# Kernel tuning notes

Hardware: AMD Instinct MI355X
Metric: run time of the kernel (lower is better)

## Reference

```python
import jax, jax.numpy as jnp
import numpy as np

L, B, S, H, NH, HD = 2, 2, 1024, 768, 12, 64
E, K, F, V = 8, 2, 3072, 50257
THETA = 10000.0
EPS = 1e-5


def setup_inputs() -> dict:
    key = jax.random.key(0)
    ks = iter(jax.random.split(key, 40))
    def nrm(shape):
        return jax.random.normal(next(ks), shape, jnp.float32) * 0.02
    return {
        "input_ids": jax.random.randint(next(ks), (B, S), 0, V),
        "emb": nrm((V, H)),
        "ln1_w": jnp.ones((L, H)), "ln1_b": jnp.zeros((L, H)),
        "ln2_w": jnp.ones((L, H)), "ln2_b": jnp.zeros((L, H)),
        "lnf_w": jnp.ones((H,)), "lnf_b": jnp.zeros((H,)),
        "Wq": nrm((L, H, H)), "bq": jnp.zeros((L, H)),
        "Wk": nrm((L, H, H)), "bk": jnp.zeros((L, H)),
        "Wv": nrm((L, H, H)), "bv": jnp.zeros((L, H)),
        "Wo": nrm((L, H, H)), "bo": jnp.zeros((L, H)),
        "Wr": nrm((L, H, E)), "br": jnp.zeros((L, E)),
        "W1": nrm((L, E, H, F)), "b1": jnp.zeros((L, E, F)),
        "W2": nrm((L, E, F, H)), "b2": jnp.zeros((L, E, H)),
    }


def _layer_norm(x, w, b):
    m = x.mean(-1, keepdims=True)
    v = ((x - m) ** 2).mean(-1, keepdims=True)
    return (x - m) * jax.lax.rsqrt(v + EPS) * w + b


def _rotate_half(x):
    x1, x2 = jnp.split(x, 2, axis=-1)
    return jnp.concatenate([-x2, x1], axis=-1)


def _forward(input_ids, emb, ln1_w, ln1_b, ln2_w, ln2_b, lnf_w, lnf_b,
             Wq, bq, Wk, bk, Wv, bv, Wo, bo, Wr, br, W1, b1, W2, b2):
    x = emb[input_ids]  # [B,S,H]

    # RoPE tables [1,1,S,HD]
    inv_freq = 1.0 / (THETA ** (jnp.arange(0, HD, 2, dtype=jnp.float32) / HD))
    freqs = jnp.arange(S, dtype=jnp.float32)[:, None] * inv_freq[None, :]
    ang = jnp.concatenate([freqs, freqs], axis=-1)
    cos = jnp.cos(ang)[None, None].astype(x.dtype)
    sin = jnp.sin(ang)[None, None].astype(x.dtype)

    causal = jnp.where(jnp.tril(jnp.ones((S, S), dtype=bool)), 0.0, -1e9)
    causal = causal[None, None].astype(x.dtype)

    scale = 1.0 / np.sqrt(HD)
    for l in range(L):
        # --- attention block ---
        h = _layer_norm(x, ln1_w[l], ln1_b[l])
        q = (h @ Wq[l] + bq[l]).reshape(B, S, NH, HD).transpose(0, 2, 1, 3)
        k = (h @ Wk[l] + bk[l]).reshape(B, S, NH, HD).transpose(0, 2, 1, 3)
        v = (h @ Wv[l] + bv[l]).reshape(B, S, NH, HD).transpose(0, 2, 1, 3)
        q = q * cos + _rotate_half(q) * sin
        k = k * cos + _rotate_half(k) * sin
        scores = jnp.einsum('bhqd,bhkd->bhqk', q, k) * scale + causal
        attn = jax.nn.softmax(scores, axis=-1)
        o = jnp.einsum('bhqk,bhkd->bhqd', attn, v)
        o = o.transpose(0, 2, 1, 3).reshape(B, S, H)
        x = x + (o @ Wo[l] + bo[l])

        # --- MoE feed-forward block ---
        h = _layer_norm(x, ln2_w[l], ln2_b[l]).reshape(-1, H)  # [N,H]
        router_probs = jax.nn.softmax(h @ Wr[l] + br[l], axis=-1)  # [N,E]
        tp, ti = jax.lax.top_k(router_probs, K)
        tp = tp / (tp.sum(-1, keepdims=True) + 1e-9)
        # combine weights per expert (equiv. to the per-slot scatter loop)
        w = (jax.nn.one_hot(ti, E, dtype=h.dtype) * tp[..., None]).sum(1)  # [N,E]
        a = jax.nn.gelu(jnp.einsum('nh,ehf->nef', h, W1[l]) + b1[l], approximate=False)
        oe = jnp.einsum('nef,efh->neh', a, W2[l]) + b2[l]
        ff = jnp.einsum('ne,neh->nh', w, oe)
        x = x + ff.reshape(B, S, H)

    x = _layer_norm(x, lnf_w, lnf_b)
    logits = jnp.einsum('bsh,vh->bsv', x, emb)  # tied lm_head
    return logits


def reference(input_ids, emb, ln1_w, ln1_b, ln2_w, ln2_b, lnf_w, lnf_b,
              Wq, bq, Wk, bk, Wv, bv, Wo, bo, Wr, br, W1, b1, W2, b2):
    return _forward(input_ids, emb, ln1_w, ln1_b, ln2_w, ln2_b, lnf_w, lnf_b,
                    Wq, bq, Wk, bk, Wv, bv, Wo, bo, Wr, br, W1, b1, W2, b2)
```

## Files before the change

### kernel.cpp

```cpp
#include <hip/hip_runtime.h>
#include <stdint.h>

constexpr int L = 2, Bb = 2, S = 1024, H = 768, NHd = 12, HD = 64;
constexpr int E = 8, F = 3072, V = 50257;
constexpr int NTOK = Bb * S;
constexpr int NSLOT = NTOK * 2;
constexpr float EPSLN = 1e-5f;

typedef __attribute__((ext_vector_type(4))) float f32x4;
typedef __attribute__((ext_vector_type(8))) short s16x8;

#define DEVI __device__ __forceinline__

DEVI float bf2f(short u) {
  union { float f; uint32_t i; } c; c.i = ((uint32_t)(uint16_t)u) << 16; return c.f;
}
DEVI short f2bf(float f) {
  union { float f; uint32_t i; } c; c.f = f;
  uint32_t x = c.i;
  uint32_t r = (x + 0x7fffu + ((x >> 16) & 1u)) >> 16;
  return (short)r;
}

DEVI void gload16(const void* g, void* l) {
  __builtin_amdgcn_global_load_lds(g, l, 16, 0, 0);
}

DEVI float gelu1(float g) { return 0.5f * g * (1.f + erff(g * 0.70710678118f)); }

__global__ void k_f32_to_bf16(const float* __restrict__ in, short* __restrict__ out, long n4) {
  long i = (long)blockIdx.x * blockDim.x + threadIdx.x;
  if (i >= n4) return;
  long base = i * 4;
  f32x4 v = *(const f32x4*)(in + base);
  short4 o;
  o.x = f2bf(v.x); o.y = f2bf(v.y); o.z = f2bf(v.z); o.w = f2bf(v.w);
  *(short4*)(out + base) = o;
}

__global__ void k_transpose_bf16(const float* __restrict__ in, short* __restrict__ out,
                                 int R, int C, long inBS, long outBS) {
  __shared__ float tile[32][33];
  const float* src = in + (size_t)blockIdx.z * inBS;
  short* dst = out + (size_t)blockIdx.z * outBS;
  int r0 = blockIdx.y * 32, c0 = blockIdx.x * 32;
  int tx = threadIdx.x, ty = threadIdx.y;
#pragma unroll
  for (int i = 0; i < 32; i += 8) {
    int r = r0 + ty + i, c = c0 + tx;
    if (r < R && c < C) tile[ty + i][tx] = src[(size_t)r * C + c];
  }
  __syncthreads();
#pragma unroll
  for (int i = 0; i < 32; i += 8) {
    int c = c0 + ty + i, r = r0 + tx;
    if (r < R && c < C) dst[(size_t)c * R + r] = f2bf(tile[tx][ty + i]);
  }
}

__global__ void k_transpose_split(const float* __restrict__ in, short* __restrict__ oh,
                                  short* __restrict__ ol, int R, int C, long inBS,
                                  long outBS) {
  __shared__ float tile[32][33];
  const float* src = in + (size_t)blockIdx.z * inBS;
  short* dh = oh + (size_t)blockIdx.z * outBS;
  short* dl = ol + (size_t)blockIdx.z * outBS;
  int r0 = blockIdx.y * 32, c0 = blockIdx.x * 32;
  int tx = threadIdx.x, ty = threadIdx.y;
#pragma unroll
  for (int i = 0; i < 32; i += 8) {
    int r = r0 + ty + i, c = c0 + tx;
    if (r < R && c < C) tile[ty + i][tx] = src[(size_t)r * C + c];
  }
  __syncthreads();
#pragma unroll
  for (int i = 0; i < 32; i += 8) {
    int c = c0 + ty + i, r = r0 + tx;
    if (r < R && c < C) {
      float v = tile[tx][ty + i];
      short hi = f2bf(v);
      short lo = f2bf(v - bf2f(hi));
      dh[(size_t)c * R + r] = hi;
      dl[(size_t)c * R + r] = lo;
    }
  }
}

__global__ void k_wqkv_t2(const float* __restrict__ Wq, const float* __restrict__ Wk,
                          const float* __restrict__ Wv, short* __restrict__ o0,
                          short* __restrict__ o1) {
  __shared__ float tile[32][33];
  const int zz = blockIdx.z;
  const float* in = (zz == 0) ? Wq : (zz == 1) ? Wk : Wv;
  const size_t doff = (size_t)zz * H * H;
  int r0 = blockIdx.y * 32, c0 = blockIdx.x * 32;
  int tx = threadIdx.x, ty = threadIdx.y;
#pragma unroll
  for (int i = 0; i < 32; i += 8) {
    int r = r0 + ty + i, c = c0 + tx;
    tile[ty + i][tx] = in[(size_t)r * H + c];
  }
  __syncthreads();
#pragma unroll
  for (int i = 0; i < 32; i += 8) {
    int c = c0 + ty + i, r = r0 + tx;
    float v = tile[tx][ty + i];
    short t0 = f2bf(v);
    short t1 = f2bf(v - bf2f(t0));
    o0[doff + (size_t)c * H + r] = t0;
    o1[doff + (size_t)c * H + r] = t1;
  }
}

__global__ void k_bqkv(const float* __restrict__ bq, const float* __restrict__ bk,
                       const float* __restrict__ bv, float* __restrict__ bqkv) {
  int i = blockIdx.x * blockDim.x + threadIdx.x;
  if (i >= L * 3 * H) return;
  int l = i / (3 * H), j = i % (3 * H);
  float v = (j < H) ? bq[l * H + j] : (j < 2 * H) ? bk[l * H + j - H] : bv[l * H + j - 2 * H];
  bqkv[i] = v;
}

__global__ void k_ropetab(float* __restrict__ cosT, float* __restrict__ sinT) {
  int i = blockIdx.x * blockDim.x + threadIdx.x;
  if (i >= S * (HD / 2)) return;
  int s = i / 32, d = i % 32;
  float invf = powf(10000.f, -(2.f * d) / (float)HD);
  float ang = (float)s * invf;
  cosT[i] = cosf(ang);
  sinT[i] = sinf(ang);
}

__global__ void k_embed(const int* __restrict__ ids, const float* __restrict__ emb,
                        float* __restrict__ x) {
  int idx = blockIdx.x * blockDim.x + threadIdx.x;
  int row = idx / (H / 4), c4 = idx % (H / 4);
  if (row >= NTOK) return;
  int t = ids[row];
  ((f32x4*)(x + (size_t)row * H))[c4] = ((const f32x4*)(emb + (size_t)t * H))[c4];
}

template <int OUT>
__global__ void k_layernorm(const float* __restrict__ x, const float* __restrict__ w,
                            const float* __restrict__ b, float* __restrict__ of,
                            short* __restrict__ s0, short* __restrict__ s1) {
  int row = blockIdx.x * (blockDim.x >> 6) + (threadIdx.x >> 6);
  int lane = threadIdx.x & 63;
  if (row >= NTOK) return;
  const float* xr = x + (size_t)row * H;
  float v[12], s = 0.f, s2s = 0.f;
#pragma unroll
  for (int j = 0; j < 12; j++) { float t = xr[lane + j * 64]; v[j] = t; s += t; s2s += t * t; }
#pragma unroll
  for (int off = 32; off; off >>= 1) { s += __shfl_xor(s, off); s2s += __shfl_xor(s2s, off); }
  float m = s / (float)H;
  float var = s2s / (float)H - m * m;
  float rs = 1.f / sqrtf(var + EPSLN);
#pragma unroll
  for (int j = 0; j < 12; j++) {
    int c = lane + j * 64;
    float val = (v[j] - m) * rs * w[c] + b[c];
    size_t idx = (size_t)row * H + c;
    if (OUT == 1) {
      short t0 = f2bf(val);
      s0[idx] = t0; s1[idx] = f2bf(val - bf2f(t0));
    } else if (OUT == 2) {
      of[idx] = val;
      short hi = f2bf(val);
      s0[idx] = hi; s1[idx] = f2bf(val - bf2f(hi));
    } else if (OUT == 3) {
      of[idx] = val;
      s0[idx] = f2bf(val);
    } else {
      s0[idx] = f2bf(val);
    }
  }
}

__global__ void k_softmax2(short* __restrict__ p0, short* __restrict__ p1) {
  int row = blockIdx.x * 4 + (threadIdx.x >> 6);
  int lane = threadIdx.x & 63;
  const int nb = ((row & (S - 1)) >> 7) + 1;
  const size_t base = (size_t)row * S;
  float v[16];
  float mx = -3e38f;
#pragma unroll
  for (int c = 0; c < 8; ++c) {
    if (c < nb) {
      uint32_t u0 = *(const uint32_t*)(p0 + base + c * 128 + lane * 2);
      uint32_t u1 = *(const uint32_t*)(p1 + base + c * 128 + lane * 2);
      float a = bf2f((short)(u0 & 0xffff)) + bf2f((short)(u1 & 0xffff));
      float b = bf2f((short)(u0 >> 16)) + bf2f((short)(u1 >> 16));
      v[c * 2] = a; v[c * 2 + 1] = b;
      mx = fmaxf(mx, fmaxf(a, b));
    }
  }
#pragma unroll
  for (int off = 32; off; off >>= 1) mx = fmaxf(mx, __shfl_xor(mx, off));
  float sum = 0.f;
#pragma unroll
  for (int c = 0; c < 8; ++c) {
    if (c < nb) {
      float a = expf(v[c * 2] - mx);
      float b = expf(v[c * 2 + 1] - mx);
      v[c * 2] = a; v[c * 2 + 1] = b;
      sum += a + b;
    }
  }
#pragma unroll
  for (int off = 32; off; off >>= 1) sum += __shfl_xor(sum, off);
  float inv = 1.f / sum;
#pragma unroll
  for (int c = 0; c < 8; ++c) {
    if (c < nb) {
      float a = v[c * 2] * inv;
      float b = v[c * 2 + 1] * inv;
      short ah = f2bf(a), bh = f2bf(b);
      short al = f2bf(a - bf2f(ah)), bl = f2bf(b - bf2f(bh));
      *(uint32_t*)(p0 + base + c * 128 + lane * 2) =
          (uint32_t)(uint16_t)ah | ((uint32_t)(uint16_t)bh << 16);
      *(uint32_t*)(p1 + base + c * 128 + lane * 2) =
          (uint32_t)(uint16_t)al | ((uint32_t)(uint16_t)bl << 16);
    }
  }
}

__global__ void k_router(const float* __restrict__ h, const float* __restrict__ Wr,
                         const float* __restrict__ br, float* __restrict__ sel_w,
                         int* __restrict__ sel_e, int* __restrict__ counts) {
  int tok = blockIdx.x * (blockDim.x >> 6) + (threadIdx.x >> 6);
  int lane = threadIdx.x & 63;
  if (tok >= NTOK) return;
  const float* hr = h + (size_t)tok * H;
  float acc[8] = {0, 0, 0, 0, 0, 0, 0, 0};
  for (int i = lane; i < H; i += 64) {
    float hv = hr[i];
    const f32x4* w4 = (const f32x4*)(Wr + (size_t)i * E);
    f32x4 a = w4[0], b = w4[1];
    acc[0] += hv * a.x; acc[1] += hv * a.y; acc[2] += hv * a.z; acc[3] += hv * a.w;
    acc[4] += hv * b.x; acc[5] += hv * b.y; acc[6] += hv * b.z; acc[7] += hv * b.w;
  }
#pragma unroll
  for (int off = 32; off; off >>= 1)
#pragma unroll
    for (int e = 0; e < 8; e++) acc[e] += __shfl_xor(acc[e], off);
  if (lane == 0) {
    float lg[8], m = -3e38f;
#pragma unroll
    for (int e = 0; e < 8; e++) { lg[e] = acc[e] + br[e]; m = fmaxf(m, lg[e]); }
    float sum = 0.f;
#pragma unroll
    for (int e = 0; e < 8; e++) { lg[e] = expf(lg[e] - m); sum += lg[e]; }
    float inv = 1.f / sum;
#pragma unroll
    for (int e = 0; e < 8; e++) lg[e] *= inv;
    int i1 = 0;
#pragma unroll
    for (int e = 1; e < 8; e++) if (lg[e] > lg[i1]) i1 = e;
    int i2 = (i1 == 0) ? 1 : 0;
#pragma unroll
    for (int e = 0; e < 8; e++) if (e != i1 && lg[e] > lg[i2]) i2 = e;
    float p1 = lg[i1], p2 = lg[i2];
    float ws = p1 + p2 + 1e-9f;
    sel_e[tok * 2] = i1; sel_e[tok * 2 + 1] = i2;
    sel_w[tok * 2] = p1 / ws; sel_w[tok * 2 + 1] = p2 / ws;
    atomicAdd(counts + i1, 1);
    atomicAdd(counts + i2, 1);
  }
}

__global__ void k_offsets(const int* __restrict__ counts, int* __restrict__ offs) {
  if (threadIdx.x == 0) {
    int a = 0;
    for (int e = 0; e < E; e++) { offs[e] = a; a += counts[e]; }
    offs[E] = a;
  }
}

__global__ void k_scatter(const int* __restrict__ sel_e, const int* __restrict__ offs,
                          int* __restrict__ cursor, int* __restrict__ tok_list,
                          int* __restrict__ slot_of) {
  int tok = blockIdx.x * blockDim.x + threadIdx.x;
  if (tok >= NTOK) return;
  for (int k = 0; k < 2; k++) {
    int e = sel_e[tok * 2 + k];
    int pos = atomicAdd(cursor + e, 1);
    int g = offs[e] + pos;
    tok_list[g] = tok;
    slot_of[tok * 2 + k] = g;
  }
}

__global__ void k_combine(const float* __restrict__ oe, const float* __restrict__ sel_w,
                          const int* __restrict__ slot_of, const int* __restrict__ sel_e,
                          const float* __restrict__ b2, float* __restrict__ x) {
  int idx = blockIdx.x * blockDim.x + threadIdx.x;
  if (idx >= NTOK * (H / 4)) return;
  int tok = idx / (H / 4), c4 = idx % (H / 4);
  float w0 = sel_w[tok * 2], w1 = sel_w[tok * 2 + 1];
  int s0 = slot_of[tok * 2], s1 = slot_of[tok * 2 + 1];
  int e0 = sel_e[tok * 2], e1 = sel_e[tok * 2 + 1];
  f32x4 a = ((const f32x4*)(oe + (size_t)s0 * H))[c4];
  f32x4 b = ((const f32x4*)(oe + (size_t)s1 * H))[c4];
  f32x4 ba = ((const f32x4*)(b2 + (size_t)e0 * H))[c4];
  f32x4 bb = ((const f32x4*)(b2 + (size_t)e1 * H))[c4];
  f32x4* xp = (f32x4*)(x + (size_t)tok * H) + c4;
  *xp = *xp + w0 * (a + ba) + w1 * (b + bb);
}

template <int SP, int MODE, bool GATHER>
__global__ __launch_bounds__(256, 2) void k_bgemmS(
    const short* __restrict__ A0, const short* __restrict__ A1, const short* __restrict__ A2,
    long sAz, int lda,
    const short* __restrict__ B0, const short* __restrict__ B1, const short* __restrict__ B2,
    long sBz, int ldb,
    void* __restrict__ Cp, void* __restrict__ Cp2,
    short* __restrict__ K0, short* __restrict__ K1,
    short* __restrict__ V0, short* __restrict__ V1,
    const float* __restrict__ cT, const float* __restrict__ sT,
    int zdiv, long sChi, long sClo, int ldc,
    const float* __restrict__ res, const float* __restrict__ bias, long sBias,
    int M, int N, int K,
    const int* __restrict__ d_counts, const int* __restrict__ d_offs,
    const int* __restrict__ gidx, float alpha) {
  const int z = blockIdx.z;
  const int Meff = d_counts ? d_counts[z] : M;
  const int tm = blockIdx.y;
  if (tm * 128 >= Meff) return;
  const int tn = blockIdx.x;
  const int row_base = d_offs ? d_offs[z] : 0;

  if (MODE == 7 && tn > tm) return;

  __shared__ short Ab[SP][128 * 32];
  __shared__ short Bb2[SP][128 * 32];

  const int tid = threadIdx.x;
  const int lane = tid & 63;
  const int w = tid >> 6;

  const int wr = (w >> 1) * 64;
  const int wc = (w & 1) * 64;
  const int r16 = lane & 15;
  const int kb4 = lane >> 4;
  const int q4 = lane >> 4;

  const short* APz[3];
  const short* BPz[3];
  APz[0] = A0 + (size_t)z * sAz;
  APz[1] = A1 + (size_t)z * sAz;
  APz[2] = (SP > 2) ? (A2 + (size_t)z * sAz) : APz[0];
  BPz[0] = B0 + (size_t)z * sBz;
  BPz[1] = B1 + (size_t)z * sBz;
  BPz[2] = (SP > 2) ? (B2 + (size_t)z * sBz) : BPz[0];

  size_t aOff[2], bOff[2];
#pragma unroll
  for (int i = 0; i < 2; ++i) {
    const int srow = i * 64 + (tid >> 2);
    const int kb = (tid & 3) ^ (srow & 3);
    int lrow = tm * 128 + srow;
    if (lrow > Meff - 1) lrow = Meff - 1;
    int ar = row_base + lrow;
    if (GATHER) ar = gidx[ar];
    aOff[i] = (size_t)ar * lda + kb * 8;
    int bcol = tn * 128 + srow;
    if (bcol > N - 1) bcol = N - 1;
    bOff[i] = (size_t)bcol * ldb + kb * 8;
  }

  f32x4 acc[4][4];
#pragma unroll
  for (int a = 0; a < 4; ++a)
#pragma unroll
    for (int b = 0; b < 4; ++b) acc[a][b] = {0.f, 0.f, 0.f, 0.f};

  const int swz = (kb4 ^ (r16 & 3)) * 8;
  int aoff[4], boff[4];
#pragma unroll
  for (int i = 0; i < 4; ++i) {
    aoff[i] = (wr + i * 16 + r16) * 32 + swz;
    boff[i] = (wc + i * 16 + r16) * 32 + swz;
  }

  const int Keff = (MODE == 8) ? (((tm + 1) * 128 < K) ? (tm + 1) * 128 : K) : K;

  for (int k0 = 0; k0 < Keff; k0 += 32) {
#pragma unroll
    for (int s = 0; s < SP; ++s) {
      gload16(APz[s] + aOff[0], (char*)(&Ab[s][0]) + w * 1024);
      gload16(APz[s] + aOff[1], (char*)(&Ab[s][0]) + 4096 + w * 1024);
      gload16(BPz[s] + bOff[0], (char*)(&Bb2[s][0]) + w * 1024);
      gload16(BPz[s] + bOff[1], (char*)(&Bb2[s][0]) + 4096 + w * 1024);
    }
    aOff[0] += 32; aOff[1] += 32; bOff[0] += 32; bOff[1] += 32;
    __syncthreads();
    s16x8 af[SP][4], bf[SP][4];
#pragma unroll
    for (int s = 0; s < SP; ++s)
#pragma unroll
      for (int i = 0; i < 4; ++i) {
        af[s][i] = *(const s16x8*)(&Ab[s][aoff[i]]);
        bf[s][i] = *(const s16x8*)(&Bb2[s][boff[i]]);
      }
#pragma unroll
    for (int mi = 0; mi < 4; ++mi)
#pragma unroll
      for (int ni = 0; ni < 4; ++ni) {
        f32x4 a = acc[mi][ni];
#pragma unroll
        for (int si = 0; si < SP; ++si)
#pragma unroll
          for (int sj = 0; sj < SP - si; ++sj)
            a = __builtin_amdgcn_mfma_f32_16x16x32_bf16(af[si][mi], bf[sj][ni], a, 0, 0, 0);
        acc[mi][ni] = a;
      }
    __syncthreads();
  }

  const float* bz = bias ? (bias + (size_t)z * sBias) : nullptr;
  float bvv[4];
  int gco[4];
#pragma unroll
  for (int ni = 0; ni < 4; ++ni) {
    gco[ni] = tn * 128 + wc + ni * 16 + r16;
    bvv[ni] = (bz && gco[ni] < N) ? bz[gco[ni]] : 0.f;
  }

  if (MODE == 9) {
    const int sec_base = tn * 128 + wc;
    const int sec = sec_base / H;
    const int hh = (sec_base % H) / HD;
#pragma unroll
    for (int mi = 0; mi < 4; ++mi) {
#pragma unroll
      for (int j = 0; j < 4; ++j) {
        const int row = tm * 128 + wr + mi * 16 + q4 * 4 + j;
        const int ss = row & (S - 1);
        const long zz = (long)((row >> 10) * NHd + hh);
#pragma unroll
        for (int ni = 0; ni < 2; ++ni) {
          const int d = ni * 16 + r16;
          float a1 = acc[mi][ni][j] + bvv[ni];
          float a2 = acc[mi][ni + 2][j] + bvv[ni + 2];
          if (sec < 2) {
            float cc = cT[ss * 32 + d], sn = sT[ss * 32 + d];
            float r1 = a1 * cc - a2 * sn;
            float r2 = a2 * cc + a1 * sn;
            const long bi = (zz * S + ss) * HD + d;
            short* d0 = (sec == 0) ? (short*)Cp : K0;
            short* d1 = (sec == 0) ? (short*)Cp2 : K1;
            short t0 = f2bf(r1);
            d0[bi] = t0; d1[bi] = f2bf(r1 - bf2f(t0));
            t0 = f2bf(r2);
            d0[bi + 32] = t0; d1[bi + 32] = f2bf(r2 - bf2f(t0));
          } else {
            const long vb1 = zz * HD * S + (long)d * S + ss;
            short hv = f2bf(a1);
            V0[vb1] = hv; V1[vb1] = f2bf(a1 - bf2f(hv));
            const long vb2 = vb1 + 32L * S;
            hv = f2bf(a2);
            V0[vb2] = hv; V1[vb2] = f2bf(a2 - bf2f(hv));
          }
        }
      }
    }
    return;
  }

  const long out_off = (long)(z / zdiv) * sChi + (long)(z % zdiv) * sClo;
#pragma unroll
  for (int mi = 0; mi < 4; ++mi) {
#pragma unroll
    for (int j = 0; j < 4; ++j) {
      const int lrow = tm * 128 + wr + mi * 16 + q4 * 4 + j;
      if (lrow >= Meff) continue;
      const long rbase = out_off + (long)(row_base + lrow) * ldc;
#pragma unroll
      for (int ni = 0; ni < 4; ++ni) {
        if (gco[ni] >= N) continue;
        const float v = acc[mi][ni][j];
        const long idx = rbase + gco[ni];
        if (MODE == 0) {
          ((float*)Cp)[idx] = v + bvv[ni];
        } else if (MODE == 1) {
          ((float*)Cp)[idx] = res[idx] + v + bvv[ni];
        } else if (MODE == 6) {
          float g = gelu1(v + bvv[ni]);
          short hi = f2bf(g);
          ((short*)Cp)[idx] = hi;
          ((short*)Cp2)[idx] = f2bf(g - bf2f(hi));
        } else if (MODE == 7) {
          float g = v * alpha + ((gco[ni] > lrow) ? -1e9f : 0.f);
          short hi = f2bf(g);
          ((short*)Cp)[idx] = hi;
          ((short*)Cp2)[idx] = f2bf(g - bf2f(hi));
        } else if (MODE == 8) {
          float g = v + bvv[ni];
          short t0 = f2bf(g);
          ((short*)Cp)[idx] = t0;
          ((short*)Cp2)[idx] = f2bf(g - bf2f(t0));
        }
      }
    }
  }
}

template <int SP, int MODE, bool GATHER>
static void bgemmS(hipStream_t st, const short* A0, const short* A1, const short* A2, long sAz,
                   int lda, const short* B0, const short* B1, const short* B2, long sBz,
                   int ldb, void* C, void* C2, int zdiv, long sChi, long sClo,
                   int ldc, const float* res, const float* bias, long sBias, int M, int N,
                   int K, int nz, const int* cnts, const int* offs_, const int* gat,
                   float alpha, short* K0 = nullptr, short* K1 = nullptr,
                   short* V0 = nullptr, short* V1 = nullptr, const float* cT = nullptr,
                   const float* sT = nullptr) {
  dim3 g((N + 127) / 128, (M + 127) / 128, nz);
  k_bgemmS<SP, MODE, GATHER><<<g, 256, 0, st>>>(A0, A1, A2, sAz, lda, B0, B1, B2, sBz, ldb, C,
                                                C2, K0, K1, V0, V1, cT, sT, zdiv, sChi,
                                                sClo, ldc, res, bias, sBias, M, N, K, cnts,
                                                offs_, gat, alpha);
}

template <int MODE, bool GATHER, bool NSWZ>
__global__ __launch_bounds__(256, 2) void k_bgemm(
    const short* __restrict__ A, long sAz, int lda,
    const short* __restrict__ Bt, long sBz, int ldb,
    void* __restrict__ Cp, int zdiv, long sChi, long sClo, int ldc,
    const float* __restrict__ bias, long sBias,
    int M, int N, int K,
    const int* __restrict__ d_counts, const int* __restrict__ d_offs,
    const int* __restrict__ gidx) {
  const int z = blockIdx.z;
  const int Meff = d_counts ? d_counts[z] : M;
  int tm, tn;
  if (NSWZ) {
    const int bid = blockIdx.y * gridDim.x + blockIdx.x;
    const int nwg = gridDim.x * gridDim.y;
    const int q = nwg >> 3, r = nwg & 7;
    const int xcd = bid & 7, ix = bid >> 3;
    const int wg = (xcd < r) ? (xcd * (q + 1) + ix) : (r * (q + 1) + (xcd - r) * q + ix);
    tn = wg / gridDim.y;
    tm = wg % gridDim.y;
  } else {
    tm = blockIdx.y;
    tn = blockIdx.x;
  }
  if (tm * 128 >= Meff) return;
  const int row_base = d_offs ? d_offs[z] : 0;

  __shared__ short Abuf[128 * 64];
  __shared__ short Bbuf[128 * 64];

  const int tid = threadIdx.x;
  const int lane = tid & 63;
  const int w = tid >> 6;

  const short* Az = A + (size_t)z * sAz;
  const short* Bz = Bt + (size_t)z * sBz;

  const int swzS = ((lane >> 3) ^ (lane & 7)) * 8;
  const short* aSrc[4];
  const short* bSrc[4];
#pragma unroll
  for (int i = 0; i < 4; ++i) {
    const int rin = (w * 4 + i) * 8 + (lane >> 3);
    int lrow = tm * 128 + rin;
    if (lrow > Meff - 1) lrow = Meff - 1;
    int ar = row_base + lrow;
    if (GATHER) ar = gidx[ar];
    aSrc[i] = Az + (size_t)ar * lda + swzS;
    int bcol = tn * 128 + rin;
    if (bcol > N - 1) bcol = N - 1;
    bSrc[i] = Bz + (size_t)bcol * ldb + swzS;
  }

  f32x4 acc[4][4];
#pragma unroll
  for (int a = 0; a < 4; ++a)
#pragma unroll
    for (int b = 0; b < 4; ++b) acc[a][b] = {0.f, 0.f, 0.f, 0.f};

  const int wr = (w >> 1) * 64;
  const int wc = (w & 1) * 64;
  const int r16 = lane & 15;
  const int kb4 = lane >> 4;
  int aoff[4][2], boff[4][2];
#pragma unroll
  for (int i = 0; i < 4; ++i) {
#pragma unroll
    for (int kw = 0; kw < 2; ++kw) {
      const int sw = ((r16 & 7) ^ (kw * 4 + kb4)) * 8;
      aoff[i][kw] = (wr + i * 16 + r16) * 64 + sw;
      boff[i][kw] = (wc + i * 16 + r16) * 64 + sw;
    }
  }

  for (int k0 = 0; k0 < K; k0 += 64) {
#pragma unroll
    for (int i = 0; i < 4; ++i) gload16(aSrc[i], (char*)Abuf + (w * 4 + i) * 1024);
#pragma unroll
    for (int i = 0; i < 4; ++i) gload16(bSrc[i], (char*)Bbuf + (w * 4 + i) * 1024);
#pragma unroll
    for (int i = 0; i < 4; ++i) { aSrc[i] += 64; bSrc[i] += 64; }
    __syncthreads();
#pragma unroll
    for (int kw = 0; kw < 2; ++kw) {
      s16x8 af[4], bf[4];
#pragma unroll
      for (int i = 0; i < 4; ++i) {
        af[i] = *(const s16x8*)(Abuf + aoff[i][kw]);
        bf[i] = *(const s16x8*)(Bbuf + boff[i][kw]);
      }
#pragma unroll
      for (int mi = 0; mi < 4; ++mi)
#pragma unroll
        for (int ni = 0; ni < 4; ++ni)
          acc[mi][ni] =
              __builtin_amdgcn_mfma_f32_16x16x32_bf16(af[mi], bf[ni], acc[mi][ni], 0, 0, 0);
    }
    __syncthreads();
  }

  const long out_off = (long)(z / zdiv) * sChi + (long)(z % zdiv) * sClo;
  const float* bz = bias ? (bias + (size_t)z * sBias) : nullptr;
  const int q4 = lane >> 4;
  float bvv[4];
  int gco[4];
#pragma unroll
  for (int ni = 0; ni < 4; ++ni) {
    gco[ni] = tn * 128 + wc + ni * 16 + r16;
    bvv[ni] = (bz && gco[ni] < N) ? bz[gco[ni]] : 0.f;
  }
#pragma unroll
  for (int mi = 0; mi < 4; ++mi) {
#pragma unroll
    for (int j = 0; j < 4; ++j) {
      const int lrow = tm * 128 + wr + mi * 16 + q4 * 4 + j;
      if (lrow >= Meff) continue;
      const long rbase = out_off + (row_base + lrow) * (long)ldc;
#pragma unroll
      for (int ni = 0; ni < 4; ++ni) {
        if (gco[ni] >= N) continue;
        const float v = acc[mi][ni][j];
        if (MODE == 0) {
          ((float*)Cp)[rbase + gco[ni]] = v + bvv[ni];
        } else if (MODE == 4) {
          float g = v + bvv[ni];
          ((short*)Cp)[rbase + gco[ni]] = f2bf(gelu1(g));
        }
      }
    }
  }
}

template <int MODE, bool GATHER, bool NSWZ>
static void bgemm(hipStream_t st, const short* A, long sAz, int lda, const short* Bt, long sBz,
                  int ldb, void* C, int zdiv, long sChi, long sClo, int ldc, const float* bias,
                  long sBias, int M, int N, int K, int nz, const int* cnts, const int* offs_,
                  const int* gat) {
  dim3 g((N + 127) / 128, (M + 127) / 128, nz);
  k_bgemm<MODE, GATHER, NSWZ><<<g, 256, 0, st>>>(A, sAz, lda, Bt, sBz, ldb, C, zdiv, sChi,
                                                 sClo, ldc, bias, sBias, M, N, K, cnts, offs_,
                                                 gat);
}

extern "C" void kernel_launch(void* const* d_in, const int* in_sizes, int n_in, void* d_out,
                              int out_size, void* d_ws, size_t ws_size, hipStream_t stream) {
  (void)in_sizes; (void)n_in; (void)out_size; (void)ws_size;
  const int*   ids  = (const int*)d_in[0];
  const float* emb  = (const float*)d_in[1];
  const float* ln1w = (const float*)d_in[2];
  const float* ln1b = (const float*)d_in[3];
  const float* ln2w = (const float*)d_in[4];
  const float* ln2b = (const float*)d_in[5];
  const float* lnfw = (const float*)d_in[6];
  const float* lnfb = (const float*)d_in[7];
  const float* Wq = (const float*)d_in[8];
  const float* bq = (const float*)d_in[9];
  const float* Wk = (const float*)d_in[10];
  const float* bk = (const float*)d_in[11];
  const float* Wv = (const float*)d_in[12];
  const float* bv = (const float*)d_in[13];
  const float* Wo = (const float*)d_in[14];
  const float* bo = (const float*)d_in[15];
  const float* Wr = (const float*)d_in[16];
  const float* br = (const float*)d_in[17];
  const float* W1 = (const float*)d_in[18];
  const float* b1 = (const float*)d_in[19];
  const float* W2 = (const float*)d_in[20];
  const float* b2 = (const float*)d_in[21];
  float* out = (float*)d_out;

  char* p = (char*)d_ws;
  auto alloc = [&](size_t bytes) {
    char* r = p;
    p += (bytes + 255) & ~(size_t)255;
    return r;
  };
  short* embB = (short*)alloc((size_t)V * H * 2);
  char* big = alloc((size_t)Bb * NHd * S * S * 2 * 2);
  short* p0   = (short*)big;
  short* p1   = p0 + (size_t)Bb * NHd * S * S;
  short* R_hi = (short*)big;
  short* R_lo = R_hi + (size_t)E * F * H;
  short* Wb0 = (short*)alloc((size_t)3 * H * H * 2);
  short* Wb1 = (short*)alloc((size_t)3 * H * H * 2);
  short* Wo0 = (short*)alloc((size_t)H * H * 2);
  short* Wo1 = (short*)alloc((size_t)H * H * 2);
  float* bqkv = (float*)alloc((size_t)L * 3 * H * 4);
  float* cosT = (float*)alloc((size_t)S * 32 * 4);
  float* sinT = (float*)alloc((size_t)S * 32 * 4);
  float* x    = (float*)alloc((size_t)NTOK * H * 4);
  float* hbuf = (float*)alloc((size_t)NTOK * H * 4);
  short* xb   = (short*)alloc((size_t)NTOK * H * 2);
  short* xb2  = (short*)alloc((size_t)NTOK * H * 2);
  short* h_hi = (short*)alloc((size_t)NTOK * H * 2);
  short* h_lo = (short*)alloc((size_t)NTOK * H * 2);
  short* h30  = (short*)alloc((size_t)NTOK * H * 2);
  short* h31  = (short*)alloc((size_t)NTOK * H * 2);
  short* q30  = (short*)alloc((size_t)NTOK * H * 2);
  short* q31  = (short*)alloc((size_t)NTOK * H * 2);
  short* k30  = (short*)alloc((size_t)NTOK * H * 2);
  short* k31  = (short*)alloc((size_t)NTOK * H * 2);
  short* v20  = (short*)alloc((size_t)NTOK * H * 2);
  short* v21  = (short*)alloc((size_t)NTOK * H * 2);
  short* o30  = (short*)alloc((size_t)NTOK * H * 2);
  short* o31  = (short*)alloc((size_t)NTOK * H * 2);
  char* uni = alloc((size_t)NSLOT * F * 4 + (size_t)NSLOT * H * 4);
  short* act_hi = (short*)uni;
  short* act_lo = (short*)(uni + (size_t)NSLOT * F * 2);
  short* act_b  = (short*)uni;
  float* oe     = (float*)(uni + (size_t)NSLOT * F * 4);
  int* counts  = (int*)alloc(2 * E * 4);
  int* cursor  = counts + E;
  int* offs    = (int*)alloc((E + 1) * 4);
  int* sel_e   = (int*)alloc((size_t)NTOK * 2 * 4);
  float* sel_w = (float*)alloc((size_t)NTOK * 2 * 4);
  int* slot_of = (int*)alloc((size_t)NTOK * 2 * 4);
  int* tok_lst = (int*)alloc((size_t)NSLOT * 4);

  long nEmb4 = (long)V * H / 4;
  k_f32_to_bf16<<<(nEmb4 + 255) / 256, 256, 0, stream>>>(emb, embB, nEmb4);
  k_bqkv<<<(L * 3 * H + 255) / 256, 256, 0, stream>>>(bq, bk, bv, bqkv);
  k_ropetab<<<(S * 32 + 255) / 256, 256, 0, stream>>>(cosT, sinT);
  k_embed<<<(NTOK * (H / 4) + 255) / 256, 256, 0, stream>>>(ids, emb, x);

  dim3 tb(32, 8);
  const dim3 tHH(H / 32, H / 32, 1);

  for (int l = 0; l < L; l++) {
    k_layernorm<1><<<NTOK / 4, 256, 0, stream>>>(x, ln1w + l * H, ln1b + l * H, nullptr, h30,
                                                 h31);
    k_wqkv_t2<<<dim3(H / 32, H / 32, 3), tb, 0, stream>>>(
        Wq + (size_t)l * H * H, Wk + (size_t)l * H * H, Wv + (size_t)l * H * H, Wb0, Wb1);
    bgemmS<2, 9, false>(stream, h30, h31, nullptr, 0, H, Wb0, Wb1, nullptr, 0, H, q30, q31,
                        1, 0, 0, 0, nullptr, bqkv + l * 3 * H, 0, NTOK, 3 * H, H, 1, nullptr,
                        nullptr, nullptr, 1.f, k30, k31, v20, v21, cosT, sinT);
    bgemmS<2, 7, false>(stream, q30, q31, nullptr, (long)S * HD, HD, k30, k31, nullptr,
                        (long)S * HD, HD, p0, p1, 1, (long)S * S, 0, S, nullptr, nullptr, 0,
                        S, S, HD, Bb * NHd, nullptr, nullptr, nullptr, 0.125f);
    k_softmax2<<<(Bb * NHd * S) / 4, 256, 0, stream>>>(p0, p1);
    bgemmS<2, 8, false>(stream, p0, p1, nullptr, (long)S * S, S, v20, v21, nullptr,
                        (long)HD * S, S, o30, o31, NHd, (long)S * H, HD, H, nullptr,
                        nullptr, 0, S, HD, S, Bb * NHd, nullptr, nullptr, nullptr, 1.f);
    k_transpose_split<<<tHH, tb, 0, stream>>>(Wo + (size_t)l * H * H, Wo0, Wo1, H, H, 0, 0);
    bgemmS<2, 1, false>(stream, o30, o31, nullptr, 0, H, Wo0, Wo1, nullptr, 0, H, x, nullptr,
                        1, 0, 0, H, x, bo + l * H, 0, NTOK, H, H, 1, nullptr, nullptr, nullptr,
                        1.f);

    if (l == 0)
      k_layernorm<2><<<NTOK / 4, 256, 0, stream>>>(x, ln2w + l * H, ln2b + l * H, hbuf, h_hi,
                                                   h_lo);
    else
      k_layernorm<3><<<NTOK / 4, 256, 0, stream>>>(x, ln2w + l * H, ln2b + l * H, hbuf, xb2,
                                                   nullptr);
    hipMemsetAsync(counts, 0, 2 * E * sizeof(int), stream);
    k_router<<<NTOK / 4, 256, 0, stream>>>(hbuf, Wr + (size_t)l * H * E, br + l * E, sel_w,
                                           sel_e, counts);
    k_offsets<<<1, 64, 0, stream>>>(counts, offs);
    k_scatter<<<(NTOK + 255) / 256, 256, 0, stream>>>(sel_e, offs, cursor, tok_lst, slot_of);
    if (l == 0) {
      k_transpose_split<<<dim3(F / 32, H / 32, E), tb, 0, stream>>>(
          W1, R_hi, R_lo, H, F, (long)H * F, (long)F * H);
      bgemmS<2, 6, true>(stream, h_hi, h_lo, nullptr, 0, H, R_hi, R_lo, nullptr, (long)F * H,
                         H, act_hi, act_lo, 1, 0, 0, F, nullptr, b1, F, NSLOT, F, H,
                         E, counts, offs, tok_lst, 1.f);
      k_transpose_split<<<dim3(H / 32, F / 32, E), tb, 0, stream>>>(
          W2, R_hi, R_lo, F, H, (long)F * H, (long)H * F);
      bgemmS<2, 0, false>(stream, act_hi, act_lo, nullptr, 0, F, R_hi, R_lo, nullptr,
                          (long)H * F, F, oe, nullptr, 1, 0, 0, H, nullptr, nullptr,
                          0, NSLOT, H, F, E, counts, offs, nullptr, 1.f);
      k_combine<<<(NTOK * (H / 4) + 255) / 256, 256, 0, stream>>>(oe, sel_w, slot_of, sel_e,
                                                                  b2, x);
    } else {
      k_transpose_bf16<<<dim3(F / 32, H / 32, E), tb, 0, stream>>>(
          W1 + (size_t)1 * E * H * F, R_hi, H, F, (long)H * F, (long)F * H);
      k_transpose_bf16<<<dim3(H / 32, F / 32, E), tb, 0, stream>>>(
          W2 + (size_t)1 * E * F * H, R_lo, F, H, (long)F * H, (long)H * F);
      bgemm<4, true, false>(stream, xb2, 0, H, R_hi, (long)F * H, H, act_b, 1, 0, 0, F,
                            b1 + (size_t)l * E * F, F, NSLOT, F, H, E, counts, offs, tok_lst);
      bgemm<0, false, false>(stream, act_b, 0, F, R_lo, (long)H * F, F, oe, 1, 0, 0, H,
                             nullptr, 0, NSLOT, H, F, E, counts, offs, nullptr);
      k_combine<<<(NTOK * (H / 4) + 255) / 256, 256, 0, stream>>>(oe, sel_w, slot_of, sel_e,
                                                                  b2 + (size_t)l * E * H, x);
    }
  }

  k_layernorm<4><<<NTOK / 4, 256, 0, stream>>>(x, lnfw, lnfb, nullptr, xb, nullptr);
  bgemm<0, false, true>(stream, xb, 0, H, embB, 0, H, out, 1, 0, 0, V, nullptr, 0, NTOK, V, H,
                        1, nullptr, nullptr, nullptr);
}
```

Measured before the change: 1.578 ms.

## Double-buffer GEMM LDS tiles with K-step 32 and async prefetch

Splits the GEMM main loop into K-chunks of 32 and keeps two LDS buffers. The next chunk's global-to-LDS loads are issued while the current chunk is computed, with explicit vmcnt waits and barriers in place of a load-then-sync pattern. The LDS swizzle is redone for the narrower tile to avoid bank conflicts. This adds more barriers per unit of K and halves the MFMA work between syncs, which may limit the overlap it gains.

```diff
diff --git a/kernel.cpp b/kernel.cpp
--- a/kernel.cpp
+++ b/kernel.cpp
@@ -549,8 +549,8 @@
   if (tm * 128 >= Meff) return;
   const int row_base = d_offs ? d_offs[z] : 0;
 
-  __shared__ short Abuf[128 * 64];
-  __shared__ short Bbuf[128 * 64];
+  __shared__ short Ab[2][128 * 32];
+  __shared__ short Bb[2][128 * 32];
 
   const int tid = threadIdx.x;
   const int lane = tid & 63;
@@ -559,20 +559,20 @@
   const short* Az = A + (size_t)z * sAz;
   const short* Bz = Bt + (size_t)z * sBz;
 
-  const int swzS = ((lane >> 3) ^ (lane & 7)) * 8;
-  const short* aSrc[4];
-  const short* bSrc[4];
-#pragma unroll
-  for (int i = 0; i < 4; ++i) {
-    const int rin = (w * 4 + i) * 8 + (lane >> 3);
+  const int srcSwz = ((lane & 3) ^ ((lane >> 2) & 3) ^ ((lane >> 4) & 3)) * 8;
+  const short* aSrc[2];
+  const short* bSrc[2];
+#pragma unroll
+  for (int i = 0; i < 2; ++i) {
+    const int rin = (w * 2 + i) * 16 + (lane >> 2);
     int lrow = tm * 128 + rin;
     if (lrow > Meff - 1) lrow = Meff - 1;
     int ar = row_base + lrow;
     if (GATHER) ar = gidx[ar];
-    aSrc[i] = Az + (size_t)ar * lda + swzS;
+    aSrc[i] = Az + (size_t)ar * lda + srcSwz;
     int bcol = tn * 128 + rin;
     if (bcol > N - 1) bcol = N - 1;
-    bSrc[i] = Bz + (size_t)bcol * ldb + swzS;
+    bSrc[i] = Bz + (size_t)bcol * ldb + srcSwz;
   }
 
   f32x4 acc[4][4];
@@ -585,41 +585,59 @@
   const int wc = (w & 1) * 64;
   const int r16 = lane & 15;
   const int kb4 = lane >> 4;
-  int aoff[4][2], boff[4][2];
+  const int fR = (r16 & 3) ^ ((r16 >> 2) & 3);
+  int aoff[4], boff[4];
 #pragma unroll
   for (int i = 0; i < 4; ++i) {
-#pragma unroll
-    for (int kw = 0; kw < 2; ++kw) {
-      const int sw = ((r16 & 7) ^ (kw * 4 + kb4)) * 8;
-      aoff[i][kw] = (wr + i * 16 + r16) * 64 + sw;
-      boff[i][kw] = (wc + i * 16 + r16) * 64 + sw;
-    }
-  }
-
-  for (int k0 = 0; k0 < K; k0 += 64) {
-#pragma unroll
-    for (int i = 0; i < 4; ++i) gload16(aSrc[i], (char*)Abuf + (w * 4 + i) * 1024);
-#pragma unroll
-    for (int i = 0; i < 4; ++i) gload16(bSrc[i], (char*)Bbuf + (w * 4 + i) * 1024);
-#pragma unroll
-    for (int i = 0; i < 4; ++i) { aSrc[i] += 64; bSrc[i] += 64; }
-    __syncthreads();
-#pragma unroll
-    for (int kw = 0; kw < 2; ++kw) {
-      s16x8 af[4], bf[4];
-#pragma unroll
-      for (int i = 0; i < 4; ++i) {
-        af[i] = *(const s16x8*)(Abuf + aoff[i][kw]);
-        bf[i] = *(const s16x8*)(Bbuf + boff[i][kw]);
-      }
-#pragma unroll
-      for (int mi = 0; mi < 4; ++mi)
-#pragma unroll
-        for (int ni = 0; ni < 4; ++ni)
-          acc[mi][ni] =
-              __builtin_amdgcn_mfma_f32_16x16x32_bf16(af[mi], bf[ni], acc[mi][ni], 0, 0, 0);
-    }
-    __syncthreads();
+    aoff[i] = (wr + i * 16 + r16) * 32 + (kb4 ^ fR) * 8;
+    boff[i] = (wc + i * 16 + r16) * 32 + (kb4 ^ fR) * 8;
+  }
+
+  auto stage = [&](int buf) {
+#pragma unroll
+    for (int i = 0; i < 2; ++i) {
+      gload16(aSrc[i], (char*)(&Ab[buf][0]) + (w * 2 + i) * 1024);
+      gload16(bSrc[i], (char*)(&Bb[buf][0]) + (w * 2 + i) * 1024);
+    }
+#pragma unroll
+    for (int i = 0; i < 2; ++i) { aSrc[i] += 32; bSrc[i] += 32; }
+  };
+  auto compute = [&](int buf) {
+    const short* Ad = &Ab[buf][0];
+    const short* Bd = &Bb[buf][0];
+    s16x8 af[4], bf[4];
+#pragma unroll
+    for (int i = 0; i < 4; ++i) {
+      af[i] = *(const s16x8*)(Ad + aoff[i]);
+      bf[i] = *(const s16x8*)(Bd + boff[i]);
+    }
+#pragma unroll
+    for (int mi = 0; mi < 4; ++mi)
+#pragma unroll
+      for (int ni = 0; ni < 4; ++ni)
+        acc[mi][ni] =
+            __builtin_amdgcn_mfma_f32_16x16x32_bf16(af[mi], bf[ni], acc[mi][ni], 0, 0, 0);
+  };
+
+  const int nt = K / 32;
+  stage(0);
+  stage(1);
+  int cur = 0;
+  for (int t = 0; t < nt; ++t) {
+    if (t + 1 < nt) {
+      asm volatile("s_waitcnt vmcnt(4)" ::: "memory");
+    } else {
+      asm volatile("s_waitcnt vmcnt(0)" ::: "memory");
+    }
+    __builtin_amdgcn_sched_barrier(0);
+    __builtin_amdgcn_s_barrier();
+    __builtin_amdgcn_sched_barrier(0);
+    compute(cur);
+    __builtin_amdgcn_sched_barrier(0);
+    __builtin_amdgcn_s_barrier();
+    __builtin_amdgcn_sched_barrier(0);
+    if (t + 2 < nt) stage(cur);
+    cur ^= 1;
   }
 
   const long out_off = (long)(z / zdiv) * sChi + (long)(z % zdiv) * sClo;
```

Result: slower. 1.627 ms (+3.1%).
